# Kernel tuning notes

Hardware: AMD Instinct MI355X
Metric: run time of the kernel (lower is better)

## Reference

```python
import jax, jax.numpy as jnp
import numpy as np

CLAMP_MIN = 1e-6
CLAMP_MAX = 1e6


def setup_inputs() -> dict:
    key = jax.random.key(0)
    k1, k2, k3, k4, k5 = jax.random.split(key, 5)
    R, F, K = 4096, 256, 8
    return {
        "x1": jax.random.normal(k1, (R, F), dtype=jnp.float32),
        "x2": jax.random.normal(k2, (R, F), dtype=jnp.float32),
        "sigmas": jax.random.normal(k3, (K,), dtype=jnp.float32) * 100.0,
        "means": jax.random.normal(k4, (K,), dtype=jnp.float32),
        "sigma_parameters": jax.random.normal(k5, (K,), dtype=jnp.float32),
    }


def reference(x1, x2, sigmas, means, sigma_parameters):
    # dist_k[i,j] = sum_f (x1[i,f] - x2[j,f] - mean_k)^2
    #            = ||x1_i - x2_j||^2 - 2*mean_k*sum_f(x1_i - x2_j) + F*mean_k^2
    # Expansion avoids materializing the R x R x F broadcast tensor.
    R, F = x1.shape
    base = (
        jnp.sum(x1 * x1, axis=1)[:, None]
        + jnp.sum(x2 * x2, axis=1)[None, :]
        - 2.0 * (x1 @ x2.T)
    )  # [R, R]
    s = jnp.sum(x1, axis=1)[:, None] - jnp.sum(x2, axis=1)[None, :]  # [R, R]

    mean = means[:, None, None]  # [K,1,1]
    dist = base[None] - 2.0 * mean * s[None] + jnp.float32(F) * mean * mean  # [K,R,R]
    dist = jnp.clip(dist, CLAMP_MIN, CLAMP_MAX)

    kernel_value = jnp.exp(-dist / (2.0 * sigmas[:, None, None] ** 2))  # [K,R,R]
    softmaxed = jax.nn.softmax(kernel_value, axis=2)  # torch softmax(dim=1) per [R,R]

    weights = 1.0 / (sigma_parameters ** 2)
    normalized_weights = jax.nn.softmax(weights)  # softmax over K
    return jnp.sum(softmaxed * normalized_weights[:, None, None], axis=0)  # [R, R]
```

## Files before the change

### kernel.cpp

```cpp
#include <hip/hip_runtime.h>
#include <cmath>

#define R 4096
#define F 256
#define NK 8

typedef _Float16 half8 __attribute__((ext_vector_type(8)));
typedef _Float16 half4v __attribute__((ext_vector_type(4)));
typedef float f32x4 __attribute__((ext_vector_type(4)));

#define LOG2E      1.4426950408889634f
#define LOG2LOG2E  0.5287663729448977f


__global__ __launch_bounds__(256) void prep_kernel(
    const float* __restrict__ x1, const float* __restrict__ x2,
    const float* __restrict__ sigmas, const float* __restrict__ means,
    const float* __restrict__ sigp,
    _Float16* __restrict__ x1h, _Float16* __restrict__ x2h,
    float* __restrict__ rA, float* __restrict__ cB,
    float* __restrict__ S, float* __restrict__ prm)
{
    const int tid  = threadIdx.x;
    const int wid  = tid >> 6;
    const int lane = tid & 63;
    const int row  = blockIdx.x * 4 + wid;

    const float* src; _Float16* dsth; int r; bool isX1;
    if (row < R) { src = x1; dsth = x1h; r = row;     isX1 = true;  }
    else         { src = x2; dsth = x2h; r = row - R; isX1 = false; }

    float4 v = ((const float4*)(src + (size_t)r * F))[lane];
    half4v h = { (_Float16)v.x, (_Float16)v.y, (_Float16)v.z, (_Float16)v.w };
    *(half4v*)(dsth + (size_t)r * F + lane * 4) = h;

    float s = v.x + v.y + v.z + v.w;
    float q = v.x * v.x + v.y * v.y + v.z * v.z + v.w * v.w;
    for (int m = 1; m < 64; m <<= 1) {
        s += __shfl_xor(s, m);
        q += __shfl_xor(q, m);
    }
    if (lane < NK) {
        int k = lane;
        float sg = sigmas[k], m = means[k];
        float c  = -LOG2E / (2.f * sg * sg);
        if (isX1) rA[k * R + r] = c * (q - 2.f * m * s + (float)F * m * m) + LOG2LOG2E;
        else      cB[k * R + r] = c * (q + 2.f * m * s);
    }

    int g = blockIdx.x * 256 + tid;
    if (g < NK * R) S[g] = 0.f;

    if (blockIdx.x == 0 && tid == 0) {
        float w[NK], mx = -1e30f;
        for (int k = 0; k < NK; ++k) { float sp = sigp[k]; w[k] = 1.f / (sp * sp); mx = fmaxf(mx, w[k]); }
        float sum = 0.f;
        for (int k = 0; k < NK; ++k) { w[k] = expf(w[k] - mx); sum += w[k]; }
        for (int k = 0; k < NK; ++k) prm[k] = w[k] / sum;
        for (int k = 0; k < NK; ++k) {
            float sg = sigmas[k];
            prm[8 + k] = LOG2E / (sg * sg);
        }
    }
}

template <int CTRL>
__device__ __forceinline__ float dpp_radd(float x) {
    int xi = __builtin_bit_cast(int, x);
    int yi = __builtin_amdgcn_update_dpp(0, xi, CTRL, 0xF, 0xF, true);
    return x + __builtin_bit_cast(float, yi);
}

__device__ __forceinline__ void gload_lds16(const void* g, void* l) {
    __builtin_amdgcn_global_load_lds(
        (const __attribute__((address_space(1))) void*)g,
        (__attribute__((address_space(3))) void*)l, 16, 0, 0);
}

#define GEMM_BODY                                                             \
    __shared__ _Float16 As[128 * 64];                                         \
    __shared__ _Float16 Bs[128 * 64];                                         \
    const int tid  = threadIdx.x;                                             \
    const int lane = tid & 63;                                                \
    const int wid  = tid >> 6;                                                \
    const int wm   = wid >> 1, wn = wid & 1;          \
    const int q    = lane >> 4, m16 = lane & 15;                              \
    const int tm   = blockIdx.y, tn = blockIdx.x;                             \
    const int srow  = tid >> 3;                        \
    const int slot  = tid & 7;                       \
    const int sslot = slot ^ (srow & 7);            \
    f32x4 acc[4][4];                                                          \
    _Pragma("unroll")                                                         \
    for (int a = 0; a < 4; ++a)                                               \
        _Pragma("unroll")                                                     \
        for (int b = 0; b < 4; ++b)                                           \
            acc[a][b] = (f32x4){0.f, 0.f, 0.f, 0.f};                          \
    for (int k0 = 0; k0 < F; k0 += 64) {                                      \
        _Pragma("unroll")                                                     \
        for (int c = 0; c < 4; ++c) {                                         \
            int row = c * 32 + srow;                                          \
            gload_lds16(&Ah[(size_t)(tm * 128 + row) * F + k0 + sslot * 8],   \
                        &As[row * 64 + slot * 8]);                            \
            gload_lds16(&Bh[(size_t)(tn * 128 + row) * F + k0 + sslot * 8],   \
                        &Bs[row * 64 + slot * 8]);                            \
        }                                                                     \
        __syncthreads();                                                      \
        _Pragma("unroll")                                                     \
        for (int s = 0; s < 2; ++s) {                                         \
            half8 a[4], b[4];                                                 \
            _Pragma("unroll")                                                 \
            for (int mt = 0; mt < 4; ++mt) {                                  \
                int ar = wm * 64 + mt * 16 + m16;                             \
                a[mt] = *(const half8*)&As[ar * 64 +                          \
                         (((s * 4 + q) ^ (ar & 7)) * 8)];                     \
            }                                                                 \
            _Pragma("unroll")                                                 \
            for (int nt = 0; nt < 4; ++nt) {                                  \
                int br = wn * 64 + nt * 16 + m16;                             \
                b[nt] = *(const half8*)&Bs[br * 64 +                          \
                         (((s * 4 + q) ^ (br & 7)) * 8)];                     \
            }                                                                 \
            _Pragma("unroll")                                                 \
            for (int mt = 0; mt < 4; ++mt)                                    \
                _Pragma("unroll")                                             \
                for (int nt = 0; nt < 4; ++nt)                                \
                    acc[mt][nt] = __builtin_amdgcn_mfma_f32_16x16x32_f16(     \
                        a[mt], b[nt], acc[mt][nt], 0, 0, 0);                  \
        }                                                                     \
        __syncthreads();                                                      \
    }

__global__ __launch_bounds__(256, 2) void gemm_phase0(
    const _Float16* __restrict__ Ah, const _Float16* __restrict__ Bh,
    const float* __restrict__ rA, const float* __restrict__ cB,
    const float* __restrict__ prm, float* __restrict__ S)
{
    GEMM_BODY

    float g[8];
#pragma unroll
    for (int k = 0; k < 8; ++k) g[k] = prm[8 + k];

    float colQ[8][4];
#pragma unroll
    for (int nt = 0; nt < 4; ++nt) {
        int colg = tn * 128 + wn * 64 + nt * 16 + m16;
#pragma unroll
        for (int k = 0; k < 8; ++k) colQ[k][nt] = cB[k * R + colg];
    }

#pragma unroll
    for (int mt = 0; mt < 4; ++mt) {
        int rowb = tm * 128 + wm * 64 + mt * 16 + q * 4;
#pragma unroll
        for (int k = 0; k < 8; ++k) {
            f32x4 ra4 = *(const f32x4*)&rA[k * R + rowb];
#pragma unroll
            for (int r = 0; r < 4; ++r) {
                float t = 0.f;
#pragma unroll
                for (int nt = 0; nt < 4; ++nt) {
                    float tt = fmaf(g[k], acc[mt][nt][r], ra4[r] + colQ[k][nt]);
                    t += __builtin_amdgcn_exp2f(__builtin_amdgcn_exp2f(tt));
                }
                t = dpp_radd<0xB1>(t);
                t = dpp_radd<0x4E>(t);
                t = dpp_radd<0x124>(t);
                t = dpp_radd<0x128>(t);
                if (m16 == 0) atomicAdd(&S[k * R + rowb + r], t);
            }
        }
    }
}

__global__ __launch_bounds__(256, 2) void gemm_phase1(
    const _Float16* __restrict__ Ah, const _Float16* __restrict__ Bh,
    const float* __restrict__ rA, const float* __restrict__ cB,
    const float* __restrict__ prm, const float* __restrict__ S,
    float* __restrict__ out)
{
    GEMM_BODY

    float g[8], wv[8];
#pragma unroll
    for (int k = 0; k < 8; ++k) { g[k] = prm[8 + k]; wv[k] = prm[k]; }

    int colg[4];
    float colQ[8][4];
#pragma unroll
    for (int nt = 0; nt < 4; ++nt) {
        colg[nt] = tn * 128 + wn * 64 + nt * 16 + m16;
#pragma unroll
        for (int k = 0; k < 8; ++k) colQ[k][nt] = cB[k * R + colg[nt]];
    }

#pragma unroll
    for (int mt = 0; mt < 4; ++mt) {
#pragma unroll
        for (int r = 0; r < 4; ++r) {
            int rowg = tm * 128 + wm * 64 + mt * 16 + q * 4 + r;
            float rAv[8];
#pragma unroll
            for (int k = 0; k < 8; ++k) rAv[k] = rA[k * R + rowg];
            float sv[8];
#pragma unroll
            for (int k = 0; k < 8; ++k)
                sv[k] = wv[k] * __builtin_amdgcn_rcpf(S[k * R + rowg]);
#pragma unroll
            for (int nt = 0; nt < 4; ++nt) {
                float d = acc[mt][nt][r];
                float o = 0.f;
#pragma unroll
                for (int k = 0; k < 8; ++k) {
                    float tt = fmaf(g[k], d, rAv[k] + colQ[k][nt]);
                    o = fmaf(sv[k], __builtin_amdgcn_exp2f(__builtin_amdgcn_exp2f(tt)), o);
                }
                out[(size_t)rowg * R + colg[nt]] = o;
            }
        }
    }
}

extern "C" void kernel_launch(void* const* d_in, const int* in_sizes, int n_in,
                              void* d_out, int out_size, void* d_ws, size_t ws_size,
                              hipStream_t stream) {
    (void)in_sizes; (void)n_in; (void)out_size; (void)ws_size;
    const float* x1     = (const float*)d_in[0];
    const float* x2     = (const float*)d_in[1];
    const float* sigmas = (const float*)d_in[2];
    const float* means  = (const float*)d_in[3];
    const float* sigp   = (const float*)d_in[4];
    float* out = (float*)d_out;

    char* ws = (char*)d_ws;
    _Float16* x1h = (_Float16*)ws;
    _Float16* x2h = (_Float16*)(ws + 2097152);
    float* S   = (float*)(ws + 4194304);
    float* rA  = (float*)(ws + 4194304 + 131072);
    float* cB  = (float*)(ws + 4194304 + 262144);
    float* prm = (float*)(ws + 4194304 + 393216);

    prep_kernel<<<2048, 256, 0, stream>>>(x1, x2, sigmas, means, sigp,
                                          x1h, x2h, rA, cB, S, prm);
    gemm_phase0<<<dim3(32, 32), 256, 0, stream>>>(x1h, x2h, rA, cB, prm, S);
    gemm_phase1<<<dim3(32, 32), 256, 0, stream>>>(x1h, x2h, rA, cB, prm, S, out);
}
```

Baseline: 186.0 us.

## Use padded LDS with register staging and vectorize epilogue row-stat loads

Measured after the change: 181.3 us. 1.03x faster.

```diff
diff --git a/kernel.cpp b/kernel.cpp
--- a/kernel.cpp
+++ b/kernel.cpp
@@ -71,24 +71,16 @@
     return x + __builtin_bit_cast(float, yi);
 }
 
-__device__ __forceinline__ void gload_lds16(const void* g, void* l) {
-    __builtin_amdgcn_global_load_lds(
-        (const __attribute__((address_space(1))) void*)g,
-        (__attribute__((address_space(3))) void*)l, 16, 0, 0);
-}
-
 #define GEMM_BODY                                                             \
-    __shared__ _Float16 As[128 * 64];                                         \
-    __shared__ _Float16 Bs[128 * 64];                                         \
+    constexpr int SK = 72;                                                    \
+    __shared__ _Float16 As[128 * SK];                                         \
+    __shared__ _Float16 Bs[128 * SK];                                         \
     const int tid  = threadIdx.x;                                             \
     const int lane = tid & 63;                                                \
     const int wid  = tid >> 6;                                                \
     const int wm   = wid >> 1, wn = wid & 1;          \
     const int q    = lane >> 4, m16 = lane & 15;                              \
     const int tm   = blockIdx.y, tn = blockIdx.x;                             \
-    const int srow  = tid >> 3;                        \
-    const int slot  = tid & 7;                       \
-    const int sslot = slot ^ (srow & 7);            \
     f32x4 acc[4][4];                                                          \
     _Pragma("unroll")                                                         \
     for (int a = 0; a < 4; ++a)                                               \
@@ -98,28 +90,25 @@
     for (int k0 = 0; k0 < F; k0 += 64) {                                      \
         _Pragma("unroll")                                                     \
         for (int c = 0; c < 4; ++c) {                                         \
-            int row = c * 32 + srow;                                          \
-            gload_lds16(&Ah[(size_t)(tm * 128 + row) * F + k0 + sslot * 8],   \
-                        &As[row * 64 + slot * 8]);                            \
-            gload_lds16(&Bh[(size_t)(tn * 128 + row) * F + k0 + sslot * 8],   \
-                        &Bs[row * 64 + slot * 8]);                            \
+            int idx = c * 256 + tid;          \
+            int row = idx >> 3, c8 = (idx & 7) * 8;                           \
+            *(uint4*)&As[row * SK + c8] =                                     \
+                *(const uint4*)&Ah[(size_t)(tm * 128 + row) * F + k0 + c8];   \
+            *(uint4*)&Bs[row * SK + c8] =                                     \
+                *(const uint4*)&Bh[(size_t)(tn * 128 + row) * F + k0 + c8];   \
         }                                                                     \
         __syncthreads();                                                      \
         _Pragma("unroll")                                                     \
         for (int s = 0; s < 2; ++s) {                                         \
             half8 a[4], b[4];                                                 \
             _Pragma("unroll")                                                 \
-            for (int mt = 0; mt < 4; ++mt) {                                  \
-                int ar = wm * 64 + mt * 16 + m16;                             \
-                a[mt] = *(const half8*)&As[ar * 64 +                          \
-                         (((s * 4 + q) ^ (ar & 7)) * 8)];                     \
-            }                                                                 \
+            for (int mt = 0; mt < 4; ++mt)                                    \
+                a[mt] = *(const half8*)&As[(wm * 64 + mt * 16 + m16) * SK +   \
+                                           s * 32 + q * 8];                   \
             _Pragma("unroll")                                                 \
-            for (int nt = 0; nt < 4; ++nt) {                                  \
-                int br = wn * 64 + nt * 16 + m16;                             \
-                b[nt] = *(const half8*)&Bs[br * 64 +                          \
-                         (((s * 4 + q) ^ (br & 7)) * 8)];                     \
-            }                                                                 \
+            for (int nt = 0; nt < 4; ++nt)                                    \
+                b[nt] = *(const half8*)&Bs[(wn * 64 + nt * 16 + m16) * SK +   \
+                                           s * 32 + q * 8];                   \
             _Pragma("unroll")                                                 \
             for (int mt = 0; mt < 4; ++mt)                                    \
                 _Pragma("unroll")                                             \
@@ -196,28 +185,36 @@
 
 #pragma unroll
     for (int mt = 0; mt < 4; ++mt) {
-#pragma unroll
-        for (int r = 0; r < 4; ++r) {
-            int rowg = tm * 128 + wm * 64 + mt * 16 + q * 4 + r;
-            float rAv[8];
-#pragma unroll
-            for (int k = 0; k < 8; ++k) rAv[k] = rA[k * R + rowg];
-            float sv[8];
-#pragma unroll
-            for (int k = 0; k < 8; ++k)
-                sv[k] = wv[k] * __builtin_amdgcn_rcpf(S[k * R + rowg]);
-#pragma unroll
-            for (int nt = 0; nt < 4; ++nt) {
-                float d = acc[mt][nt][r];
-                float o = 0.f;
-#pragma unroll
-                for (int k = 0; k < 8; ++k) {
-                    float tt = fmaf(g[k], d, rAv[k] + colQ[k][nt]);
-                    o = fmaf(sv[k], __builtin_amdgcn_exp2f(__builtin_amdgcn_exp2f(tt)), o);
+        int rowb = tm * 128 + wm * 64 + mt * 16 + q * 4;
+
+        float o[4][4];
+#pragma unroll
+        for (int r = 0; r < 4; ++r)
+#pragma unroll
+            for (int nt = 0; nt < 4; ++nt) o[r][nt] = 0.f;
+
+#pragma unroll
+        for (int k = 0; k < 8; ++k) {
+            f32x4 ra4 = *(const f32x4*)&rA[k * R + rowb];
+            f32x4 s4  = *(const f32x4*)&S[k * R + rowb];
+#pragma unroll
+            for (int r = 0; r < 4; ++r) {
+                float sv = wv[k] * __builtin_amdgcn_rcpf(s4[r]);
+#pragma unroll
+                for (int nt = 0; nt < 4; ++nt) {
+                    float tt = fmaf(g[k], acc[mt][nt][r], ra4[r] + colQ[k][nt]);
+                    o[r][nt] = fmaf(sv,
+                        __builtin_amdgcn_exp2f(__builtin_amdgcn_exp2f(tt)),
+                        o[r][nt]);
                 }
-                out[(size_t)rowg * R + colg[nt]] = o;
             }
         }
+
+#pragma unroll
+        for (int r = 0; r < 4; ++r)
+#pragma unroll
+            for (int nt = 0; nt < 4; ++nt)
+                out[(size_t)(rowb + r) * R + colg[nt]] = o[r][nt];
     }
 }
 
```
